# Kernel tuning notes

Hardware: AMD Instinct MI355X
Metric: run time of the kernel (lower is better)

Reference implementation:

```python
import jax, jax.numpy as jnp
import numpy as np
import math

EPS = 1e-5

def conv1x1(x, w):
    # x: (B,C,H,W), w: (O,C)
    return jnp.einsum('bchw,oc->bohw', x, w)

def bn(x, gamma, beta, mean, var):
    # inference-mode batchnorm, params shape (C,)
    s = (gamma / jnp.sqrt(var + EPS))[None, :, None, None]
    b = (beta - mean * gamma / jnp.sqrt(var + EPS))[None, :, None, None]
    return x * s + b

def setup_inputs() -> dict:
    key = jax.random.key(0)
    ks = jax.random.split(key, 16)
    B, C1, C2, OUT, W, H = 4, 256, 64, 64, 64, 64
    inp = {
        'rgb': jax.random.normal(ks[0], (B, C2, W, H), jnp.float32),
        'dep': jax.random.normal(ks[1], (B, C1, W, H), jnp.float32),
        # dep fusion conv (1x1) + BN
        'conv_w': jax.random.normal(ks[2], (C2, C1), jnp.float32) * (1.0 / np.sqrt(C1)),
        'bn1_g': jax.random.uniform(ks[3], (C2,), jnp.float32, 0.5, 1.5),
        'bn1_b': jax.random.normal(ks[4], (C2,), jnp.float32) * 0.1,
        'bn1_m': jax.random.normal(ks[5], (C2,), jnp.float32) * 0.1,
        'bn1_v': jax.random.uniform(ks[6], (C2,), jnp.float32, 0.5, 1.5),
        # attention projections (1x1, no bias)
        'rgb_w': jax.random.normal(ks[7], (C2, C2), jnp.float32) * (1.0 / np.sqrt(C2)),
        'dep_w': jax.random.normal(ks[8], (C2, C2), jnp.float32) * (1.0 / np.sqrt(C2)),
        # mlp: ConvBNReLU(C2,24,1) then ConvBNSig(24,OUT,1)
        'mlp1_w': jax.random.normal(ks[9], (24, C2), jnp.float32) * (1.0 / np.sqrt(C2)),
        'bn2_g': jax.random.uniform(ks[10], (24,), jnp.float32, 0.5, 1.5),
        'bn2_b': jax.random.normal(ks[11], (24,), jnp.float32) * 0.1,
        'bn2_m': jax.random.normal(ks[12], (24,), jnp.float32) * 0.1,
        'bn2_v': jax.random.uniform(ks[13], (24,), jnp.float32, 0.5, 1.5),
        'mlp2_w': jax.random.normal(ks[14], (OUT, 24), jnp.float32) * (1.0 / np.sqrt(24)),
        'bn3_g': jax.random.uniform(jax.random.fold_in(key, 20), (OUT,), jnp.float32, 0.5, 1.5),
        'bn3_b': jax.random.normal(jax.random.fold_in(key, 21), (OUT,), jnp.float32) * 0.1,
        'bn3_m': jax.random.normal(jax.random.fold_in(key, 22), (OUT,), jnp.float32) * 0.1,
        'bn3_v': jax.random.uniform(jax.random.fold_in(key, 23), (OUT,), jnp.float32, 0.5, 1.5),
    }
    return inp

def reference(rgb, dep, conv_w, bn1_g, bn1_b, bn1_m, bn1_v, rgb_w, dep_w,
              mlp1_w, bn2_g, bn2_b, bn2_m, bn2_v, mlp2_w, bn3_g, bn3_b, bn3_m, bn3_v):
    # dep = ConvBNReLU(dep)
    dep = jax.nn.relu(bn(conv1x1(dep, conv_w), bn1_g, bn1_b, bn1_m, bn1_v))
    rgbd = rgb + dep
    B, C, W, H = rgb.shape
    N = W * H
    proj_rgb = conv1x1(rgb, rgb_w).reshape(B, C, N)  # (B,C,N)
    proj_dep = conv1x1(dep, dep_w).reshape(B, C, N)  # (B,C,N)
    # energy[b,i,j] = <proj_rgb[:,i], proj_dep[:,j]> / sqrt(C)
    energy = jnp.einsum('bci,bcj->bij', proj_rgb, proj_dep) / math.sqrt(C)
    attn = jax.nn.softmax(energy, axis=1)  # torch Softmax(dim=1): over rows i
    att_r = jnp.einsum('bci,bij->bcj', proj_rgb, attn)
    att_b = jnp.einsum('bci,bij->bcj', proj_dep, attn)
    output = (att_r + att_b).reshape(B, C, W, H) + rgbd
    gap = output.mean(axis=(2, 3), keepdims=True)  # (B,C,1,1)
    h = jax.nn.relu(bn(conv1x1(gap, mlp1_w), bn2_g, bn2_b, bn2_m, bn2_v))
    gate = jax.nn.sigmoid(bn(conv1x1(h, mlp2_w), bn3_g, bn3_b, bn3_m, bn3_v))
    return gate
```

## Files before the change

kernel.cpp:

```cpp
#include <hip/hip_runtime.h>
#include <hip/hip_bf16.h>


typedef __bf16 bf16;
typedef __bf16 bf16x4 __attribute__((ext_vector_type(4)));
typedef __bf16 bf16x8 __attribute__((ext_vector_type(8)));
typedef float  f32x4  __attribute__((ext_vector_type(4)));
typedef float  float4v __attribute__((ext_vector_type(4)));
typedef short  s4     __attribute__((ext_vector_type(4)));

#define MFMA_BF16(a, b, c) __builtin_amdgcn_mfma_f32_16x16x32_bf16((a), (b), (c), 0, 0, 0)

#if defined(__has_builtin)
# if __has_builtin(__builtin_amdgcn_mfma_f32_16x16x16bf16_1k)
#  define MFMA16_BUILTIN(a, b, c) __builtin_amdgcn_mfma_f32_16x16x16bf16_1k((a), (b), (c), 0, 0, 0)
# elif __has_builtin(__builtin_amdgcn_mfma_f32_16x16x16_bf16)
#  define MFMA16_BUILTIN(a, b, c) __builtin_amdgcn_mfma_f32_16x16x16_bf16((a), (b), (c), 0, 0, 0)
# endif
#endif

__device__ __forceinline__ f32x4 MFMA16(s4 a, s4 b, f32x4 c) {
#ifdef MFMA16_BUILTIN
    return MFMA16_BUILTIN(a, b, c);
#else
    asm("v_mfma_f32_16x16x16_bf16 %0, %1, %2, %0" : "+v"(c) : "v"(a), "v"(b));
    return c;
#endif
}

#if defined(__has_builtin)
# if __has_builtin(__builtin_amdgcn_exp2f)
#  define EXP2(x) __builtin_amdgcn_exp2f(x)
# else
#  define EXP2(x) exp2f(x)
# endif
#else
# define EXP2(x) exp2f(x)
#endif

#define K_E 0.18033688f

__device__ __forceinline__ int swz128(int row, int colByte) {
    return row * 128 + (colByte ^ ((row & 7) << 4));
}
__device__ __forceinline__ int swz512(int row, int colByte) {
    return row * 512 + (colByte ^ ((row & 15) << 4));
}

#define OW_W   0
#define OW_WR  32768
#define OW_WD  40960
#define OT_C   0
#define OT_R   16384
#define OT_D   20480
#define O_S1   49152
#define O_B1   49408
#define O_RED  49664
#define SMEMA  51712

__global__ __launch_bounds__(512, 2) void k_front(
    const float* __restrict__ rgb, const float* __restrict__ dep,
    const float* __restrict__ conv_w,
    const float* __restrict__ bn1_g, const float* __restrict__ bn1_b,
    const float* __restrict__ bn1_m, const float* __restrict__ bn1_v,
    const float* __restrict__ rgb_w, const float* __restrict__ dep_w,
    bf16* __restrict__ prF, bf16* __restrict__ pdF, bf16* __restrict__ pvF,
    float* __restrict__ rgbdPart, int* __restrict__ counter)
{
    const int bid = blockIdx.x;
    const int xcd = bid & 7;
    const int b    = xcd >> 1;
    const int tile = ((bid >> 3) << 1) | (xcd & 1);
    const int p0   = tile * 32;
    const int tid = threadIdx.x;
    const int w   = tid >> 6;
    const int lane = tid & 63;
    const int l15 = lane & 15;
    const int lg  = lane >> 4;
    const int ot4 = w & 3;
    const int ot  = ot4 * 16;
    const int ph  = w >> 2;

    if (bid == 0 && tid == 0) *counter = 0;

    __shared__ __align__(16) unsigned char smem[SMEMA];
    float* s1 = (float*)(smem + O_S1);
    float* b1 = (float*)(smem + O_B1);
    float* red = (float*)(smem + O_RED);

    {
        unsigned char* ldsW  = smem + OW_W;
        unsigned char* ldsWR = smem + OW_WR;
        unsigned char* ldsWD = smem + OW_WD;
        #pragma unroll
        for (int q = 0; q < 8; ++q) {
            const int idx = (q * 512 + tid) * 4;
            float4v v = *(const float4v*)(conv_w + idx);
            const int o = idx >> 8, c = idx & 255;
            bf16x4 h;
            #pragma unroll
            for (int j = 0; j < 4; ++j) h[j] = (bf16)v[j];
            *(bf16x4*)(ldsW + swz512(o, c * 2)) = h;
        }
        #pragma unroll
        for (int q = 0; q < 2; ++q) {
            const int idx = (q * 512 + tid) * 4;
            const int o = idx >> 6, c = idx & 63;
            float4v v = *(const float4v*)(rgb_w + idx);
            bf16x4 h;
            #pragma unroll
            for (int j = 0; j < 4; ++j) h[j] = (bf16)v[j];
            *(bf16x4*)(ldsWR + swz128(o, c * 2)) = h;
            v = *(const float4v*)(dep_w + idx);
            #pragma unroll
            for (int j = 0; j < 4; ++j) h[j] = (bf16)v[j];
            *(bf16x4*)(ldsWD + swz128(o, c * 2)) = h;
        }
        if (tid < 64) {
            float sc = bn1_g[tid] * rsqrtf(bn1_v[tid] + 1e-5f);
            s1[tid] = sc;
            b1[tid] = bn1_b[tid] - bn1_m[tid] * sc;
        }
    }
    __syncthreads();

    bf16x8 aW[8], aR[2], aD[2];
    {
        const unsigned char* ldsW  = smem + OW_W;
        const unsigned char* ldsWR = smem + OW_WR;
        const unsigned char* ldsWD = smem + OW_WD;
        const int row = ot + l15;
        #pragma unroll
        for (int kk = 0; kk < 8; ++kk)
            aW[kk] = *(const bf16x8*)(ldsW + swz512(row, (kk * 32 + lg * 8) * 2));
        #pragma unroll
        for (int kk = 0; kk < 2; ++kk) {
            aR[kk] = *(const bf16x8*)(ldsWR + swz128(row, (kk * 32 + lg * 8) * 2));
            aD[kk] = *(const bf16x8*)(ldsWD + swz128(row, (kk * 32 + lg * 8) * 2));
        }
    }
    __syncthreads();

    unsigned char* ldsC = smem + OT_C;
    unsigned char* ldsR = smem + OT_R;
    unsigned char* ldsD = smem + OT_D;
    const float* depb = dep + (size_t)b * 256 * 4096;
    const float* rgbb = rgb + (size_t)b * 64 * 4096;
    {
        const int c0 = tid >> 3, seg = tid & 7;
        #pragma unroll
        for (int r = 0; r < 4; ++r) {
            const int c = r * 64 + c0;
            float4v v = *(const float4v*)(depb + (size_t)c * 4096 + p0 + seg * 4);
            #pragma unroll
            for (int k = 0; k < 4; ++k)
                *(bf16*)(ldsC + swz512(seg * 4 + k, c * 2)) = (bf16)v[k];
        }
        float4v v = *(const float4v*)(rgbb + (size_t)c0 * 4096 + p0 + seg * 4);
        #pragma unroll
        for (int k = 0; k < 4; ++k)
            *(bf16*)(ldsR + swz128(seg * 4 + k, c0 * 2)) = (bf16)v[k];
    }
    __syncthreads();

    const int prow = ph * 16 + l15;
    f32x4 acc = {0.f, 0.f, 0.f, 0.f};
    #pragma unroll
    for (int kk = 0; kk < 8; ++kk) {
        bf16x8 bF = *(const bf16x8*)(ldsC + swz512(prow, (kk * 32 + lg * 8) * 2));
        acc = MFMA_BF16(aW[kk], bF, acc);
    }
    {
        const int o0 = ot + lg * 4;
        bf16x4 v4;
        #pragma unroll
        for (int r = 0; r < 4; ++r) {
            float x = acc[r] * s1[o0 + r] + b1[o0 + r];
            v4[r] = (bf16)(x > 0.f ? x : 0.f);
        }
        *(bf16x4*)(ldsD + swz128(prow, o0 * 2)) = v4;
    }
    __syncthreads();

    f32x4 accR = {0.f, 0.f, 0.f, 0.f}, accD = {0.f, 0.f, 0.f, 0.f};
    #pragma unroll
    for (int kk = 0; kk < 2; ++kk) {
        const int cb = (kk * 32 + lg * 8) * 2;
        bf16x8 bR = *(const bf16x8*)(ldsR + swz128(prow, cb));
        bf16x8 bD = *(const bf16x8*)(ldsD + swz128(prow, cb));
        accR = MFMA_BF16(aR[kk], bR, accR);
        accD = MFMA_BF16(aD[kk], bD, accD);
    }
    {
        const int o0 = ot + lg * 4;
        const size_t itile = (size_t)tile * 2 + ph;
        const size_t fbase = (size_t)b * 262144 + itile * 1024;
        const size_t prOff = fbase + (size_t)(o0 >> 3) * 128 + l15 * 8 + (o0 & 7);
        bf16x4 vR, vD;
        #pragma unroll
        for (int r = 0; r < 4; ++r) {
            vR[r] = (bf16)(accR[r] * K_E);
            vD[r] = (bf16)accD[r];
        }
        *(bf16x4*)(prF + prOff) = vR;
        *(bf16x4*)(pdF + prOff) = vD;
        const size_t pvBase = fbase + ot4 * 256 + (l15 >> 2) * 64 + lg * 16 + (l15 & 3);
        #pragma unroll
        for (int r = 0; r < 4; ++r)
            pvF[pvBase + r * 4] = (bf16)(accR[r] + accD[r]);
    }

    {
        const int c = tid & 63, g8 = tid >> 6;
        float sum = 0.f;
        #pragma unroll
        for (int q = 0; q < 4; ++q) {
            const int pp = g8 * 4 + q;
            sum += (float)*(const bf16*)(ldsR + swz128(pp, c * 2))
                 + (float)*(const bf16*)(ldsD + swz128(pp, c * 2));
        }
        red[g8 * 64 + c] = sum;
    }
    __syncthreads();
    if (tid < 64) {
        float s = 0.f;
        #pragma unroll
        for (int g = 0; g < 8; ++g) s += red[g * 64 + tid];
        rgbdPart[((size_t)b * 128 + tile) * 64 + tid] = s;
    }
}

#define LOADSET(A0, A1, V0, V1, V2, V3, q)                                    \
    {                                                                         \
        const bf16* pA_ = prb + (size_t)((q) * 8 + ih) * 1024;                \
        const bf16* pV_ = pvb + (size_t)((q) * 8 + ih) * 1024;                \
        A0 = *(const bf16x8*)(pA_ + lane * 8);                                \
        A1 = *(const bf16x8*)(pA_ + 512 + lane * 8);                          \
        V0 = *(const bf16x4*)(pV_ + lane * 4);                                \
        V1 = *(const bf16x4*)(pV_ + 256 + lane * 4);                          \
        V2 = *(const bf16x4*)(pV_ + 512 + lane * 4);                          \
        V3 = *(const bf16x4*)(pV_ + 768 + lane * 4);                          \
    }

#define COMPUTESET(A0, A1, V0, V1, V2, V3)                                    \
    {                                                                         \
        _Pragma("unroll")                                                     \
        for (int jt = 0; jt < 4; ++jt) {                                      \
            f32x4 e = {0.f, 0.f, 0.f, 0.f};                                   \
            e = MFMA_BF16(A0, B0[jt], e);                                     \
            e = MFMA_BF16(A1, B1[jt], e);                                     \
            bf16x4 ph_;                                                       \
            _Pragma("unroll")                                                 \
            for (int r = 0; r < 4; ++r) {                                     \
                float pf_ = EXP2(e[r]);                                       \
                z[jt] += pf_;                                                 \
                ph_[r] = (bf16)pf_;                                           \
            }                                                                 \
            const s4 pB_ = __builtin_bit_cast(s4, ph_);                       \
            acc[jt][0] = MFMA16(__builtin_bit_cast(s4, V0), pB_, acc[jt][0]); \
            acc[jt][1] = MFMA16(__builtin_bit_cast(s4, V1), pB_, acc[jt][1]); \
            acc[jt][2] = MFMA16(__builtin_bit_cast(s4, V2), pB_, acc[jt][2]); \
            acc[jt][3] = MFMA16(__builtin_bit_cast(s4, V3), pB_, acc[jt][3]); \
        }                                                                     \
    }

__global__ __launch_bounds__(512, 2) void k_col(
    const bf16* __restrict__ prF, const bf16* __restrict__ pdF,
    const bf16* __restrict__ pvF,
    float* __restrict__ gapPart, const float* __restrict__ rgbdPart,
    int* __restrict__ counter,
    const float* __restrict__ mlp1_w,
    const float* __restrict__ bn2_g, const float* __restrict__ bn2_b,
    const float* __restrict__ bn2_m, const float* __restrict__ bn2_v,
    const float* __restrict__ mlp2_w,
    const float* __restrict__ bn3_g, const float* __restrict__ bn3_b,
    const float* __restrict__ bn3_m, const float* __restrict__ bn3_v,
    float* __restrict__ out)
{
    const int bid = blockIdx.x;
    const int xcd = bid & 7, b = xcd >> 1;
    const int jt64 = ((bid >> 3) << 1) | (xcd & 1);
    const int tid = threadIdx.x;
    const int ih = tid >> 6, lane = tid & 63;
    const int l15 = lane & 15, lg = lane >> 4;

    __shared__ float zred[8][64];
    __shared__ float zfull[64];
    __shared__ float gred[8][64];
    __shared__ float gv4[4][64];
    __shared__ float h4[4][24];
    __shared__ int winflag;
    if (tid == 0) winflag = 0;

    const bf16* prb = prF + (size_t)b * 262144;
    const bf16* pdb = pdF + (size_t)b * 262144;
    const bf16* pvb = pvF + (size_t)b * 262144;

    bf16x8 B0[4], B1[4];
    #pragma unroll
    for (int jt = 0; jt < 4; ++jt) {
        const bf16* q = pdb + (size_t)(jt64 * 4 + jt) * 1024 + lane * 8;
        B0[jt] = *(const bf16x8*)q;
        B1[jt] = *(const bf16x8*)(q + 512);
    }

    f32x4 acc[4][4];
    #pragma unroll
    for (int jt = 0; jt < 4; ++jt)
        #pragma unroll
        for (int cb = 0; cb < 4; ++cb)
            acc[jt][cb] = (f32x4){0.f, 0.f, 0.f, 0.f};
    float z[4] = {0.f, 0.f, 0.f, 0.f};

    bf16x8 a0A, a1A, a0B, a1B;
    bf16x4 v0A, v1A, v2A, v3A, v0B, v1B, v2B, v3B;
    LOADSET(a0A, a1A, v0A, v1A, v2A, v3A, 0);
    LOADSET(a0B, a1B, v0B, v1B, v2B, v3B, 1);

    for (int t = 0; t < 32; t += 2) {
        COMPUTESET(a0A, a1A, v0A, v1A, v2A, v3A);
        if (t + 2 < 32) LOADSET(a0A, a1A, v0A, v1A, v2A, v3A, t + 2);
        COMPUTESET(a0B, a1B, v0B, v1B, v2B, v3B);
        if (t + 3 < 32) LOADSET(a0B, a1B, v0B, v1B, v2B, v3B, t + 3);
    }

    #pragma unroll
    for (int jt = 0; jt < 4; ++jt) {
        float zv = z[jt];
        zv += __shfl_xor(zv, 16);
        zv += __shfl_xor(zv, 32);
        if (lane < 16) zred[ih][jt * 16 + lane] = zv;
    }
    __syncthreads();
    if (tid < 64) {
        float s = 0.f;
        #pragma unroll
        for (int k = 0; k < 8; ++k) s += zred[k][tid];
        zfull[tid] = s;
    }
    __syncthreads();

    float zinv[4];
    #pragma unroll
    for (int jt = 0; jt < 4; ++jt) {
        const float zj = zfull[jt * 16 + l15];
        float zi = __builtin_amdgcn_rcpf(zj);
        zinv[jt] = zi * (2.0f - zj * zi);
    }
    #pragma unroll
    for (int cb = 0; cb < 4; ++cb) {
        #pragma unroll
        for (int r = 0; r < 4; ++r) {
            float v = acc[0][cb][r] * zinv[0] + acc[1][cb][r] * zinv[1]
                    + acc[2][cb][r] * zinv[2] + acc[3][cb][r] * zinv[3];
            v += __shfl_xor(v, 1);
            v += __shfl_xor(v, 2);
            v += __shfl_xor(v, 4);
            v += __shfl_xor(v, 8);
            if (l15 == 0) gred[ih][cb * 16 + lg * 4 + r] = v;
        }
    }
    __syncthreads();
    if (tid < 64) {
        float s = 0.f;
        #pragma unroll
        for (int k = 0; k < 8; ++k) s += gred[k][tid];
        gapPart[((size_t)b * 64 + jt64) * 64 + tid] = s;
        __threadfence();
        int old = atomicAdd(counter, 1);
        if (old == 256 * 64 - 1) winflag = 1;
    }
    __syncthreads();

    if (winflag) {
        __threadfence();
        const int wb = ih >> 1, half = ih & 1;
        float acc2 = 0.f;
        const float* gp = gapPart + ((size_t)wb * 64 + half * 32) * 64 + lane;
        #pragma unroll 4
        for (int r = 0; r < 32; ++r) acc2 += gp[r * 64];
        const float* rp = rgbdPart + ((size_t)wb * 128 + half * 64) * 64 + lane;
        #pragma unroll 4
        for (int r = 0; r < 64; ++r) acc2 += rp[r * 64];
        gred[ih][lane] = acc2;
        __syncthreads();
        if (tid < 256) {
            const int b4 = tid >> 6, c = tid & 63;
            gv4[b4][c] = (gred[2 * b4][c] + gred[2 * b4 + 1][c]) * (1.f / 4096.f);
        }
        __syncthreads();
        if (tid < 96) {
            const int b4 = tid / 24, o = tid % 24;
            float a = 0.f;
            #pragma unroll
            for (int cc = 0; cc < 64; ++cc) a += mlp1_w[o * 64 + cc] * gv4[b4][cc];
            float sc = bn2_g[o] * rsqrtf(bn2_v[o] + 1e-5f);
            a = a * sc + bn2_b[o] - bn2_m[o] * sc;
            h4[b4][o] = a > 0.f ? a : 0.f;
        }
        __syncthreads();
        if (tid < 256) {
            const int b4 = tid >> 6, c = tid & 63;
            float u = 0.f;
            #pragma unroll
            for (int o = 0; o < 24; ++o) u += mlp2_w[c * 24 + o] * h4[b4][o];
            float sc = bn3_g[c] * rsqrtf(bn3_v[c] + 1e-5f);
            u = u * sc + bn3_b[c] - bn3_m[c] * sc;
            out[b4 * 64 + c] = 1.f / (1.f + __expf(-u));
        }
    }
}

extern "C" void kernel_launch(void* const* d_in, const int* in_sizes, int n_in,
                              void* d_out, int out_size, void* d_ws, size_t ws_size,
                              hipStream_t stream)
{
    const float* rgb    = (const float*)d_in[0];
    const float* dep    = (const float*)d_in[1];
    const float* conv_w = (const float*)d_in[2];
    const float* bn1_g  = (const float*)d_in[3];
    const float* bn1_b  = (const float*)d_in[4];
    const float* bn1_m  = (const float*)d_in[5];
    const float* bn1_v  = (const float*)d_in[6];
    const float* rgb_w  = (const float*)d_in[7];
    const float* dep_w  = (const float*)d_in[8];
    const float* mlp1_w = (const float*)d_in[9];
    const float* bn2_g  = (const float*)d_in[10];
    const float* bn2_b  = (const float*)d_in[11];
    const float* bn2_m  = (const float*)d_in[12];
    const float* bn2_v  = (const float*)d_in[13];
    const float* mlp2_w = (const float*)d_in[14];
    const float* bn3_g  = (const float*)d_in[15];
    const float* bn3_b  = (const float*)d_in[16];
    const float* bn3_m  = (const float*)d_in[17];
    const float* bn3_v  = (const float*)d_in[18];

    char* ws = (char*)d_ws;
    bf16*  prF      = (bf16*)(ws);
    bf16*  pdF      = (bf16*)(ws + (2u << 20));
    bf16*  pvF      = (bf16*)(ws + (4u << 20));
    float* rgbdPart = (float*)(ws + (6u << 20));
    float* gapPart  = (float*)(ws + (6u << 20) + (128u << 10));
    int*   counter  = (int*)  (ws + (6u << 20) + (192u << 10));

    k_front<<<512, 512, 0, stream>>>(rgb, dep, conv_w,
                                     bn1_g, bn1_b, bn1_m, bn1_v,
                                     rgb_w, dep_w,
                                     prF, pdF, pvF, rgbdPart, counter);
    k_col<<<256, 512, 0, stream>>>(prF, pdF, pvF, gapPart, rgbdPart, counter,
                                   mlp1_w, bn2_g, bn2_b, bn2_m, bn2_v,
                                   mlp2_w, bn3_g, bn3_b, bn3_m, bn3_v,
                                   (float*)d_out);
}
```

Baseline: 55.04 us.

## Halve per-block column tile in attention kernel, double grid, repack V for wide loads

```diff
diff --git a/kernel.cpp b/kernel.cpp
--- a/kernel.cpp
+++ b/kernel.cpp
@@ -45,6 +45,12 @@
 }
 __device__ __forceinline__ int swz512(int row, int colByte) {
     return row * 512 + (colByte ^ ((row & 15) << 4));
+}
+__device__ __forceinline__ bf16x4 lo8(bf16x8 x) {
+    bf16x4 r; r[0] = x[0]; r[1] = x[1]; r[2] = x[2]; r[3] = x[3]; return r;
+}
+__device__ __forceinline__ bf16x4 hi8(bf16x8 x) {
+    bf16x4 r; r[0] = x[4]; r[1] = x[5]; r[2] = x[6]; r[3] = x[7]; return r;
 }
 
 #define OW_W   0
@@ -204,10 +210,11 @@
         }
         *(bf16x4*)(prF + prOff) = vR;
         *(bf16x4*)(pdF + prOff) = vD;
-        const size_t pvBase = fbase + ot4 * 256 + (l15 >> 2) * 64 + lg * 16 + (l15 & 3);
+        const size_t pvBase = fbase + (ot4 >> 1) * 512 + (l15 >> 2) * 128
+                            + lg * 32 + (ot4 & 1) * 4 + (l15 & 3);
         #pragma unroll
         for (int r = 0; r < 4; ++r)
-            pvF[pvBase + r * 4] = (bf16)(accR[r] + accD[r]);
+            pvF[pvBase + r * 8] = (bf16)(accR[r] + accD[r]);
     }
 
     {
@@ -230,22 +237,24 @@
     }
 }
 
-#define LOADSET(A0, A1, V0, V1, V2, V3, q)                                    \
+#define LOADSET(A0, A1, V01, V23, q)                                          \
     {                                                                         \
         const bf16* pA_ = prb + (size_t)((q) * 8 + ih) * 1024;                \
         const bf16* pV_ = pvb + (size_t)((q) * 8 + ih) * 1024;                \
-        A0 = *(const bf16x8*)(pA_ + lane * 8);                                \
-        A1 = *(const bf16x8*)(pA_ + 512 + lane * 8);                          \
-        V0 = *(const bf16x4*)(pV_ + lane * 4);                                \
-        V1 = *(const bf16x4*)(pV_ + 256 + lane * 4);                          \
-        V2 = *(const bf16x4*)(pV_ + 512 + lane * 4);                          \
-        V3 = *(const bf16x4*)(pV_ + 768 + lane * 4);                          \
-    }
-
-#define COMPUTESET(A0, A1, V0, V1, V2, V3)                                    \
+        A0  = *(const bf16x8*)(pA_ + lane * 8);                               \
+        A1  = *(const bf16x8*)(pA_ + 512 + lane * 8);                         \
+        V01 = *(const bf16x8*)(pV_ + lane * 8);                               \
+        V23 = *(const bf16x8*)(pV_ + 512 + lane * 8);                         \
+    }
+
+#define COMPUTESET(A0, A1, V01, V23)                                          \
     {                                                                         \
+        const s4 v0_ = __builtin_bit_cast(s4, lo8(V01));                      \
+        const s4 v1_ = __builtin_bit_cast(s4, hi8(V01));                      \
+        const s4 v2_ = __builtin_bit_cast(s4, lo8(V23));                      \
+        const s4 v3_ = __builtin_bit_cast(s4, hi8(V23));                      \
         _Pragma("unroll")                                                     \
-        for (int jt = 0; jt < 4; ++jt) {                                      \
+        for (int jt = 0; jt < 2; ++jt) {                                      \
             f32x4 e = {0.f, 0.f, 0.f, 0.f};                                   \
             e = MFMA_BF16(A0, B0[jt], e);                                     \
             e = MFMA_BF16(A1, B1[jt], e);                                     \
@@ -257,14 +266,14 @@
                 ph_[r] = (bf16)pf_;                                           \
             }                                                                 \
             const s4 pB_ = __builtin_bit_cast(s4, ph_);                       \
-            acc[jt][0] = MFMA16(__builtin_bit_cast(s4, V0), pB_, acc[jt][0]); \
-            acc[jt][1] = MFMA16(__builtin_bit_cast(s4, V1), pB_, acc[jt][1]); \
-            acc[jt][2] = MFMA16(__builtin_bit_cast(s4, V2), pB_, acc[jt][2]); \
-            acc[jt][3] = MFMA16(__builtin_bit_cast(s4, V3), pB_, acc[jt][3]); \
+            acc[jt][0] = MFMA16(v0_, pB_, acc[jt][0]);                        \
+            acc[jt][1] = MFMA16(v1_, pB_, acc[jt][1]);                        \
+            acc[jt][2] = MFMA16(v2_, pB_, acc[jt][2]);                        \
+            acc[jt][3] = MFMA16(v3_, pB_, acc[jt][3]);                        \
         }                                                                     \
     }
 
-__global__ __launch_bounds__(512, 2) void k_col(
+__global__ __launch_bounds__(512, 4) void k_col(
     const bf16* __restrict__ prF, const bf16* __restrict__ pdF,
     const bf16* __restrict__ pvF,
     float* __restrict__ gapPart, const float* __restrict__ rgbdPart,
@@ -279,13 +288,13 @@
 {
     const int bid = blockIdx.x;
     const int xcd = bid & 7, b = xcd >> 1;
-    const int jt64 = ((bid >> 3) << 1) | (xcd & 1);
+    const int jc = ((bid >> 3) << 1) | (xcd & 1);
     const int tid = threadIdx.x;
     const int ih = tid >> 6, lane = tid & 63;
     const int l15 = lane & 15, lg = lane >> 4;
 
-    __shared__ float zred[8][64];
-    __shared__ float zfull[64];
+    __shared__ float zred[8][32];
+    __shared__ float zfull[32];
     __shared__ float gred[8][64];
     __shared__ float gv4[4][64];
     __shared__ float h4[4][24];
@@ -296,43 +305,42 @@
     const bf16* pdb = pdF + (size_t)b * 262144;
     const bf16* pvb = pvF + (size_t)b * 262144;
 
-    bf16x8 B0[4], B1[4];
-    #pragma unroll
-    for (int jt = 0; jt < 4; ++jt) {
-        const bf16* q = pdb + (size_t)(jt64 * 4 + jt) * 1024 + lane * 8;
+    bf16x8 B0[2], B1[2];
+    #pragma unroll
+    for (int jt = 0; jt < 2; ++jt) {
+        const bf16* q = pdb + (size_t)(jc * 2 + jt) * 1024 + lane * 8;
         B0[jt] = *(const bf16x8*)q;
         B1[jt] = *(const bf16x8*)(q + 512);
     }
 
-    f32x4 acc[4][4];
-    #pragma unroll
-    for (int jt = 0; jt < 4; ++jt)
+    f32x4 acc[2][4];
+    #pragma unroll
+    for (int jt = 0; jt < 2; ++jt)
         #pragma unroll
         for (int cb = 0; cb < 4; ++cb)
             acc[jt][cb] = (f32x4){0.f, 0.f, 0.f, 0.f};
-    float z[4] = {0.f, 0.f, 0.f, 0.f};
-
-    bf16x8 a0A, a1A, a0B, a1B;
-    bf16x4 v0A, v1A, v2A, v3A, v0B, v1B, v2B, v3B;
-    LOADSET(a0A, a1A, v0A, v1A, v2A, v3A, 0);
-    LOADSET(a0B, a1B, v0B, v1B, v2B, v3B, 1);
+    float z[2] = {0.f, 0.f};
+
+    bf16x8 a0A, a1A, v01A, v23A, a0B, a1B, v01B, v23B;
+    LOADSET(a0A, a1A, v01A, v23A, 0);
+    LOADSET(a0B, a1B, v01B, v23B, 1);
 
     for (int t = 0; t < 32; t += 2) {
-        COMPUTESET(a0A, a1A, v0A, v1A, v2A, v3A);
-        if (t + 2 < 32) LOADSET(a0A, a1A, v0A, v1A, v2A, v3A, t + 2);
-        COMPUTESET(a0B, a1B, v0B, v1B, v2B, v3B);
-        if (t + 3 < 32) LOADSET(a0B, a1B, v0B, v1B, v2B, v3B, t + 3);
-    }
-
-    #pragma unroll
-    for (int jt = 0; jt < 4; ++jt) {
+        COMPUTESET(a0A, a1A, v01A, v23A);
+        if (t + 2 < 32) LOADSET(a0A, a1A, v01A, v23A, t + 2);
+        COMPUTESET(a0B, a1B, v01B, v23B);
+        if (t + 3 < 32) LOADSET(a0B, a1B, v01B, v23B, t + 3);
+    }
+
+    #pragma unroll
+    for (int jt = 0; jt < 2; ++jt) {
         float zv = z[jt];
         zv += __shfl_xor(zv, 16);
         zv += __shfl_xor(zv, 32);
         if (lane < 16) zred[ih][jt * 16 + lane] = zv;
     }
     __syncthreads();
-    if (tid < 64) {
+    if (tid < 32) {
         float s = 0.f;
         #pragma unroll
         for (int k = 0; k < 8; ++k) s += zred[k][tid];
@@ -340,9 +348,9 @@
     }
     __syncthreads();
 
-    float zinv[4];
-    #pragma unroll
-    for (int jt = 0; jt < 4; ++jt) {
+    float zinv[2];
+    #pragma unroll
+    for (int jt = 0; jt < 2; ++jt) {
         const float zj = zfull[jt * 16 + l15];
         float zi = __builtin_amdgcn_rcpf(zj);
         zinv[jt] = zi * (2.0f - zj * zi);
@@ -351,8 +359,7 @@
     for (int cb = 0; cb < 4; ++cb) {
         #pragma unroll
         for (int r = 0; r < 4; ++r) {
-            float v = acc[0][cb][r] * zinv[0] + acc[1][cb][r] * zinv[1]
-                    + acc[2][cb][r] * zinv[2] + acc[3][cb][r] * zinv[3];
+            float v = acc[0][cb][r] * zinv[0] + acc[1][cb][r] * zinv[1];
             v += __shfl_xor(v, 1);
             v += __shfl_xor(v, 2);
             v += __shfl_xor(v, 4);
@@ -365,10 +372,10 @@
         float s = 0.f;
         #pragma unroll
         for (int k = 0; k < 8; ++k) s += gred[k][tid];
-        gapPart[((size_t)b * 64 + jt64) * 64 + tid] = s;
+        gapPart[((size_t)b * 128 + jc) * 64 + tid] = s;
         __threadfence();
         int old = atomicAdd(counter, 1);
-        if (old == 256 * 64 - 1) winflag = 1;
+        if (old == 512 * 64 - 1) winflag = 1;
     }
     __syncthreads();
 
@@ -376,9 +383,9 @@
         __threadfence();
         const int wb = ih >> 1, half = ih & 1;
         float acc2 = 0.f;
-        const float* gp = gapPart + ((size_t)wb * 64 + half * 32) * 64 + lane;
+        const float* gp = gapPart + ((size_t)wb * 128 + half * 64) * 64 + lane;
         #pragma unroll 4
-        for (int r = 0; r < 32; ++r) acc2 += gp[r * 64];
+        for (int r = 0; r < 64; ++r) acc2 += gp[r * 64];
         const float* rp = rgbdPart + ((size_t)wb * 128 + half * 64) * 64 + lane;
         #pragma unroll 4
         for (int r = 0; r < 64; ++r) acc2 += rp[r * 64];
@@ -441,13 +448,13 @@
     bf16*  pvF      = (bf16*)(ws + (4u << 20));
     float* rgbdPart = (float*)(ws + (6u << 20));
     float* gapPart  = (float*)(ws + (6u << 20) + (128u << 10));
-    int*   counter  = (int*)  (ws + (6u << 20) + (192u << 10));
+    int*   counter  = (int*)  (ws + (6u << 20) + (256u << 10));
 
     k_front<<<512, 512, 0, stream>>>(rgb, dep, conv_w,
                                      bn1_g, bn1_b, bn1_m, bn1_v,
                                      rgb_w, dep_w,
                                      prF, pdF, pvF, rgbdPart, counter);
-    k_col<<<256, 512, 0, stream>>>(prF, pdF, pvF, gapPart, rgbdPart, counter,
+    k_col<<<512, 512, 0, stream>>>(prF, pdF, pvF, gapPart, rgbdPart, counter,
                                    mlp1_w, bn2_g, bn2_b, bn2_m, bn2_v,
                                    mlp2_w, bn3_g, bn3_b, bn3_m, bn3_v,
                                    (float*)d_out);
```

After: 58.75 us. 1.07x slower.

## Stream attention operands through LDS ring via async global_load_lds double buffering

Applied to the files above, without the earlier changes.

```diff
diff --git a/kernel.cpp b/kernel.cpp
--- a/kernel.cpp
+++ b/kernel.cpp
@@ -45,6 +45,18 @@
 }
 __device__ __forceinline__ int swz512(int row, int colByte) {
     return row * 512 + (colByte ^ ((row & 15) << 4));
+}
+__device__ __forceinline__ bf16x4 lo8(bf16x8 x) {
+    bf16x4 r; r[0] = x[0]; r[1] = x[1]; r[2] = x[2]; r[3] = x[3]; return r;
+}
+__device__ __forceinline__ bf16x4 hi8(bf16x8 x) {
+    bf16x4 r; r[0] = x[4]; r[1] = x[5]; r[2] = x[6]; r[3] = x[7]; return r;
+}
+
+__device__ __forceinline__ void gload_lds16(const void* g, void* l) {
+    __builtin_amdgcn_global_load_lds(
+        (const __attribute__((address_space(1))) void*)g,
+        (__attribute__((address_space(3))) void*)l, 16, 0, 0);
 }
 
 #define OW_W   0
@@ -204,10 +216,11 @@
         }
         *(bf16x4*)(prF + prOff) = vR;
         *(bf16x4*)(pdF + prOff) = vD;
-        const size_t pvBase = fbase + ot4 * 256 + (l15 >> 2) * 64 + lg * 16 + (l15 & 3);
+        const size_t pvBase = fbase + (ot4 >> 1) * 512 + (l15 >> 2) * 128
+                            + lg * 32 + (ot4 & 1) * 4 + (l15 & 3);
         #pragma unroll
         for (int r = 0; r < 4; ++r)
-            pvF[pvBase + r * 4] = (bf16)(accR[r] + accD[r]);
+            pvF[pvBase + r * 8] = (bf16)(accR[r] + accD[r]);
     }
 
     {
@@ -230,20 +243,32 @@
     }
 }
 
-#define LOADSET(A0, A1, V0, V1, V2, V3, q)                                    \
+#define STAGE(st, sl)                                                         \
     {                                                                         \
-        const bf16* pA_ = prb + (size_t)((q) * 8 + ih) * 1024;                \
-        const bf16* pV_ = pvb + (size_t)((q) * 8 + ih) * 1024;                \
-        A0 = *(const bf16x8*)(pA_ + lane * 8);                                \
-        A1 = *(const bf16x8*)(pA_ + 512 + lane * 8);                          \
-        V0 = *(const bf16x4*)(pV_ + lane * 4);                                \
-        V1 = *(const bf16x4*)(pV_ + 256 + lane * 4);                          \
-        V2 = *(const bf16x4*)(pV_ + 512 + lane * 4);                          \
-        V3 = *(const bf16x4*)(pV_ + 768 + lane * 4);                          \
-    }
-
-#define COMPUTESET(A0, A1, V0, V1, V2, V3)                                    \
+        const unsigned char* gp_ = prbB + (size_t)(st) * 16384 + w * 2048     \
+                                 + lane * 16;                                 \
+        unsigned char* lp_ = ring + (sl) * 32768 + w * 2048;                  \
+        gload_lds16(gp_, lp_);                                                \
+        gload_lds16(gp_ + 1024, lp_ + 1024);                                  \
+        const unsigned char* gv_ = pvbB + (size_t)(st) * 16384 + w * 2048     \
+                                 + lane * 16;                                 \
+        unsigned char* lv_ = ring + (sl) * 32768 + 16384 + w * 2048;          \
+        gload_lds16(gv_, lv_);                                                \
+        gload_lds16(gv_ + 1024, lv_ + 1024);                                  \
+    }
+
+#define COMPUTESET(sl)                                                        \
     {                                                                         \
+        const unsigned char* prS_ = ring + (sl) * 32768 + w * 2048;           \
+        const unsigned char* pvS_ = ring + (sl) * 32768 + 16384 + w * 2048;   \
+        bf16x8 A0 = *(const bf16x8*)(prS_ + lane * 16);                       \
+        bf16x8 A1 = *(const bf16x8*)(prS_ + 1024 + lane * 16);                \
+        bf16x8 V01 = *(const bf16x8*)(pvS_ + lane * 16);                      \
+        bf16x8 V23 = *(const bf16x8*)(pvS_ + 1024 + lane * 16);               \
+        const s4 v0_ = __builtin_bit_cast(s4, lo8(V01));                      \
+        const s4 v1_ = __builtin_bit_cast(s4, hi8(V01));                      \
+        const s4 v2_ = __builtin_bit_cast(s4, lo8(V23));                      \
+        const s4 v3_ = __builtin_bit_cast(s4, hi8(V23));                      \
         _Pragma("unroll")                                                     \
         for (int jt = 0; jt < 4; ++jt) {                                      \
             f32x4 e = {0.f, 0.f, 0.f, 0.f};                                   \
@@ -257,12 +282,16 @@
                 ph_[r] = (bf16)pf_;                                           \
             }                                                                 \
             const s4 pB_ = __builtin_bit_cast(s4, ph_);                       \
-            acc[jt][0] = MFMA16(__builtin_bit_cast(s4, V0), pB_, acc[jt][0]); \
-            acc[jt][1] = MFMA16(__builtin_bit_cast(s4, V1), pB_, acc[jt][1]); \
-            acc[jt][2] = MFMA16(__builtin_bit_cast(s4, V2), pB_, acc[jt][2]); \
-            acc[jt][3] = MFMA16(__builtin_bit_cast(s4, V3), pB_, acc[jt][3]); \
+            acc[jt][0] = MFMA16(v0_, pB_, acc[jt][0]);                        \
+            acc[jt][1] = MFMA16(v1_, pB_, acc[jt][1]);                        \
+            acc[jt][2] = MFMA16(v2_, pB_, acc[jt][2]);                        \
+            acc[jt][3] = MFMA16(v3_, pB_, acc[jt][3]);                        \
         }                                                                     \
     }
+
+#define WAIT_VM4   asm volatile("s_waitcnt vmcnt(4)" ::: "memory")
+#define WAIT_VM0   asm volatile("s_waitcnt vmcnt(0)" ::: "memory")
+#define WAIT_LGKM0 asm volatile("s_waitcnt lgkmcnt(0)" ::: "memory")
 
 __global__ __launch_bounds__(512, 2) void k_col(
     const bf16* __restrict__ prF, const bf16* __restrict__ pdF,
@@ -281,9 +310,10 @@
     const int xcd = bid & 7, b = xcd >> 1;
     const int jt64 = ((bid >> 3) << 1) | (xcd & 1);
     const int tid = threadIdx.x;
-    const int ih = tid >> 6, lane = tid & 63;
+    const int w = tid >> 6, lane = tid & 63;
     const int l15 = lane & 15, lg = lane >> 4;
 
+    __shared__ __align__(16) unsigned char ring[65536];
     __shared__ float zred[8][64];
     __shared__ float zfull[64];
     __shared__ float gred[8][64];
@@ -295,6 +325,8 @@
     const bf16* prb = prF + (size_t)b * 262144;
     const bf16* pdb = pdF + (size_t)b * 262144;
     const bf16* pvb = pvF + (size_t)b * 262144;
+    const unsigned char* prbB = (const unsigned char*)prb;
+    const unsigned char* pvbB = (const unsigned char*)pvb;
 
     bf16x8 B0[4], B1[4];
     #pragma unroll
@@ -312,24 +344,23 @@
             acc[jt][cb] = (f32x4){0.f, 0.f, 0.f, 0.f};
     float z[4] = {0.f, 0.f, 0.f, 0.f};
 
-    bf16x8 a0A, a1A, a0B, a1B;
-    bf16x4 v0A, v1A, v2A, v3A, v0B, v1B, v2B, v3B;
-    LOADSET(a0A, a1A, v0A, v1A, v2A, v3A, 0);
-    LOADSET(a0B, a1B, v0B, v1B, v2B, v3B, 1);
-
-    for (int t = 0; t < 32; t += 2) {
-        COMPUTESET(a0A, a1A, v0A, v1A, v2A, v3A);
-        if (t + 2 < 32) LOADSET(a0A, a1A, v0A, v1A, v2A, v3A, t + 2);
-        COMPUTESET(a0B, a1B, v0B, v1B, v2B, v3B);
-        if (t + 3 < 32) LOADSET(a0B, a1B, v0B, v1B, v2B, v3B, t + 3);
-    }
+    STAGE(0, 0);
+    STAGE(1, 1);
+    for (int t = 0; t < 30; ++t) {
+        WAIT_VM4;
+        COMPUTESET(t & 1);
+        WAIT_LGKM0;
+        STAGE(t + 2, t & 1);
+    }
+    WAIT_VM4;  COMPUTESET(0);
+    WAIT_VM0;  COMPUTESET(1);
 
     #pragma unroll
     for (int jt = 0; jt < 4; ++jt) {
         float zv = z[jt];
         zv += __shfl_xor(zv, 16);
         zv += __shfl_xor(zv, 32);
-        if (lane < 16) zred[ih][jt * 16 + lane] = zv;
+        if (lane < 16) zred[w][jt * 16 + lane] = zv;
     }
     __syncthreads();
     if (tid < 64) {
@@ -357,7 +388,7 @@
             v += __shfl_xor(v, 2);
             v += __shfl_xor(v, 4);
             v += __shfl_xor(v, 8);
-            if (l15 == 0) gred[ih][cb * 16 + lg * 4 + r] = v;
+            if (l15 == 0) gred[w][cb * 16 + lg * 4 + r] = v;
         }
     }
     __syncthreads();
@@ -374,7 +405,7 @@
 
     if (winflag) {
         __threadfence();
-        const int wb = ih >> 1, half = ih & 1;
+        const int wb = w >> 1, half = w & 1;
         float acc2 = 0.f;
         const float* gp = gapPart + ((size_t)wb * 64 + half * 32) * 64 + lane;
         #pragma unroll 4
@@ -382,7 +413,7 @@
         const float* rp = rgbdPart + ((size_t)wb * 128 + half * 64) * 64 + lane;
         #pragma unroll 4
         for (int r = 0; r < 64; ++r) acc2 += rp[r * 64];
-        gred[ih][lane] = acc2;
+        gred[w][lane] = acc2;
         __syncthreads();
         if (tid < 256) {
             const int b4 = tid >> 6, c = tid & 63;
```

Result: faster. 53.02 us (-3.7%).
